# Performance work log

Measured on AMD Instinct MI355X. Metric: run time of the kernel, lower is better.

The kernel has to match this reference:

```python
import jax, jax.numpy as jnp
import numpy as np

NUM_STAB = 0.001  # numerical_stabilizer from relu_kernel_transformation


def relu_kernel(data, proj):
    """ReLU random-feature kernel: data [B,L,H,D], proj [M,D] -> [B,L,H,M]."""
    ratio = 1.0 / jnp.sqrt(jnp.asarray(proj.shape[0], jnp.float32))
    data_dash = ratio * jnp.einsum('blhd,md->blhm', data, proj)
    return jax.nn.relu(data_dash) + NUM_STAB


def setup_inputs() -> dict:
    key = jax.random.key(0)
    k1, k2, k3, k4 = jax.random.split(key, 4)
    B, L, H, D, M = 2, 4096, 8, 64, 256
    return {
        'query': jax.random.normal(k1, (B, L, H, D), jnp.float32),
        'key_t': jax.random.normal(k2, (B, L, H, D), jnp.float32),
        'value': jax.random.normal(k3, (B, L, H, D), jnp.float32),
        'projection_matrix': jax.random.normal(k4, (M, D), jnp.float32),
    }


def reference(query, key_t, value, projection_matrix):
    # Kernel feature maps [B,L,H,M]
    qp = relu_kernel(query, projection_matrix)
    kp = relu_kernel(key_t, projection_matrix)
    # Causal path operates in [L,B,H,*] layout
    qs = jnp.transpose(qp, (1, 0, 2, 3))     # [L,B,H,M]
    ks = jnp.transpose(kp, (1, 0, 2, 3))     # [L,B,H,M]
    vs = jnp.transpose(value, (1, 0, 2, 3))  # [L,B,H,D]

    B, H, M = qs.shape[1], qs.shape[2], qs.shape[3]
    D = vs.shape[3]
    init = (jnp.zeros((B, H, M, D), qs.dtype),  # running sum of k outer v
            jnp.zeros((B, H, M), qs.dtype))     # running sum of k

    def step(carry, inp):
        kv_sum, k_sum = carry
        q, k, v = inp  # [B,H,M], [B,H,M], [B,H,D]
        kv_sum = kv_sum + k[..., None] * v[..., None, :]
        k_sum = k_sum + k
        num = jnp.einsum('bhmd,bhm->bhd', kv_sum, q)  # causal numerator step
        den = jnp.einsum('bhm,bhm->bh', q, k_sum)     # causal denominator step
        return (kv_sum, k_sum), (num, den)

    _, (num, den) = jax.lax.scan(step, init, (qs, ks, vs))  # num [L,B,H,D], den [L,B,H]
    den = den[..., None]
    den = jnp.where(den <= 0.0, jnp.ones_like(den), den)
    out = num / den                      # [L,B,H,D]
    return jnp.transpose(out, (1, 0, 2, 3))  # [B,L,H,D]
```

## Files before the change

### kernel.cpp

```cpp
#include <hip/hip_runtime.h>
#include <hip/hip_bf16.h>


#define B_   2
#define L_   4096
#define H_   8
#define D_   64
#define M_   256
#define T_   128
#define C_   (L_ / T_)
#define NBH  (B_ * H_)
#define RATIO 0.0625f
#define STAB  0.001f
#define SVT  136
#define SQS  72

typedef __attribute__((ext_vector_type(8))) short short8;
typedef __attribute__((ext_vector_type(4))) float floatx4;

#define MFMA16(a, b, c) __builtin_amdgcn_mfma_f32_16x16x32_bf16(a, b, c, 0, 0, 0)

__device__ inline unsigned short f2bf(float x) {
    union { float f; unsigned u; } v; v.f = x;
    unsigned r = v.u + 0x7FFF + ((v.u >> 16) & 1);
    return (unsigned short)(r >> 16);
}
__device__ inline float bf2f(unsigned short b) {
    union { unsigned u; float f; } v; v.u = ((unsigned)b) << 16; return v.f;
}
__device__ inline unsigned pack2bf(float a, float b) {
    __hip_bfloat162 h = __float22bfloat162_rn(make_float2(a, b));
    unsigned u; __builtin_memcpy(&u, &h, 4);
    return u;
}
__device__ inline short8 ldg8_bf(const float* p) {
    float4 a = *(const float4*)p;
    float4 b = *(const float4*)(p + 4);
    short8 r;
    r[0] = (short)f2bf(a.x); r[1] = (short)f2bf(a.y);
    r[2] = (short)f2bf(a.z); r[3] = (short)f2bf(a.w);
    r[4] = (short)f2bf(b.x); r[5] = (short)f2bf(b.y);
    r[6] = (short)f2bf(b.z); r[7] = (short)f2bf(b.w);
    return r;
}
__device__ inline short8 ldg8_bfs(const float* p) {
    float4 a = *(const float4*)p;
    float4 b = *(const float4*)(p + 4);
    short8 r;
    r[0] = (short)f2bf(a.x * RATIO); r[1] = (short)f2bf(a.y * RATIO);
    r[2] = (short)f2bf(a.z * RATIO); r[3] = (short)f2bf(a.w * RATIO);
    r[4] = (short)f2bf(b.x * RATIO); r[5] = (short)f2bf(b.y * RATIO);
    r[6] = (short)f2bf(b.z * RATIO); r[7] = (short)f2bf(b.w * RATIO);
    return r;
}

__global__ __launch_bounds__(512, 2)
void phase1_kernel(const float* __restrict__ key, const float* __restrict__ val,
                   const float* __restrict__ proj,
                   unsigned short* __restrict__ S, float* __restrict__ Z) {
    const int c = blockIdx.x, bh = blockIdx.y;
    const int b = bh / H_, h = bh % H_;
    const int tid = threadIdx.x;
    const int w = tid >> 6, lane = tid & 63;
    const int l15 = lane & 15, quad = lane >> 4;

    __shared__ __align__(16) unsigned short VT[64 * SVT];
    __shared__ __align__(16) unsigned short KpT[128 * SVT];
    __shared__ float zP[8][M_];

    const size_t rowstr = H_ * D_;
    const size_t base = ((size_t)b * L_ + (size_t)c * T_) * rowstr + (size_t)h * D_;

    for (int i = tid; i < T_ * 16; i += 512) {
        int t = i >> 4, d4 = (i & 15) * 4;
        float4 vv = *(const float4*)(val + base + (size_t)t * rowstr + d4);
        VT[(d4 + 0) * SVT + t] = f2bf(vv.x);
        VT[(d4 + 1) * SVT + t] = f2bf(vv.y);
        VT[(d4 + 2) * SVT + t] = f2bf(vv.z);
        VT[(d4 + 3) * SVT + t] = f2bf(vv.w);
    }
    short8 kf[2];
#pragma unroll
    for (int kk = 0; kk < 2; ++kk)
        kf[kk] = ldg8_bfs(key + base + (size_t)(16 * w + l15) * rowstr + kk * 32 + quad * 8);

    const int dtile = w & 3, mq = w >> 2;
    short8 vf[4];
    unsigned short* Sp = S + (size_t)(bh * C_ + c) * (M_ * D_);

    for (int hh = 0; hh < 2; ++hh) {
#pragma unroll
        for (int fgl = 0; fgl < 2; ++fgl) {
            const int fg = 2 * hh + fgl;
#pragma unroll
            for (int ct = 0; ct < 4; ++ct) {
                short8 pf0 = ldg8_bf(proj + (size_t)(fg * 64 + ct * 16 + l15) * D_ + quad * 8);
                short8 pf1 = ldg8_bf(proj + (size_t)(fg * 64 + ct * 16 + l15) * D_ + 32 + quad * 8);
                floatx4 a = {0.f, 0.f, 0.f, 0.f};
                a = MFMA16(kf[0], pf0, a);
                a = MFMA16(kf[1], pf1, a);
                const int mloc = fgl * 64 + ct * 16 + l15;
                float k0 = fmaxf(a[0], 0.f) + STAB;
                float k1 = fmaxf(a[1], 0.f) + STAB;
                float k2 = fmaxf(a[2], 0.f) + STAB;
                float k3 = fmaxf(a[3], 0.f) + STAB;
                uint2 pk; pk.x = pack2bf(k0, k1); pk.y = pack2bf(k2, k3);
                *(uint2*)&KpT[mloc * SVT + 16 * w + quad * 4] = pk;
                float zrow = (k0 + k1) + (k2 + k3);
                zrow += __shfl_xor(zrow, 16, 64);
                zrow += __shfl_xor(zrow, 32, 64);
                if (quad == 0) zP[w][hh * 128 + mloc] = zrow;
            }
        }
        __syncthreads();
        if (hh == 0) {
#pragma unroll
            for (int k4 = 0; k4 < 4; ++k4)
                vf[k4] = *(const short8*)&VT[(16 * dtile + l15) * SVT + k4 * 32 + quad * 8];
        }
#pragma unroll
        for (int ct2 = 0; ct2 < 4; ++ct2) {
            const int mrow = mq * 64 + ct2 * 16 + l15;
            floatx4 acc = {0.f, 0.f, 0.f, 0.f};
#pragma unroll
            for (int k4 = 0; k4 < 4; ++k4) {
                short8 kb = *(const short8*)&KpT[mrow * SVT + k4 * 32 + quad * 8];
                acc = MFMA16(vf[k4], kb, acc);
            }
#pragma unroll
            for (int r = 0; r < 4; ++r)
                Sp[(size_t)(16 * dtile + quad * 4 + r) * M_
                   + hh * 128 + mq * 64 + ct2 * 16 + l15] = f2bf(acc[r]);
        }
        __syncthreads();
    }
    if (tid < M_) {
        float z = 0.f;
#pragma unroll
        for (int ww = 0; ww < 8; ++ww) z += zP[ww][tid];
        Z[(size_t)(bh * C_ + c) * M_ + tid] = z;
    }
}

__global__ __launch_bounds__(256, 4)
void phase2_kernel(unsigned int* __restrict__ S2, float* __restrict__ Z) {
    const int bh = blockIdx.y;
    const int j = blockIdx.x * 256 + threadIdx.x;
    const int NP = M_ * D_ / 2;
    if (j < NP) {
        unsigned int* p = S2 + (size_t)bh * C_ * NP + j;
        unsigned int v[C_];
#pragma unroll
        for (int c = 0; c < C_; ++c) v[c] = p[(size_t)c * NP];
        float r0 = 0.f, r1 = 0.f;
#pragma unroll
        for (int c = 0; c < C_; ++c) {
            unsigned int t = v[c];
            p[(size_t)c * NP] = pack2bf(r0, r1);
            r0 += bf2f((unsigned short)(t & 0xffff));
            r1 += bf2f((unsigned short)(t >> 16));
        }
    } else {
        const int j2 = j - NP;
        if (j2 < M_) {
            float* pz = Z + (size_t)bh * C_ * M_ + j2;
            float v[C_];
#pragma unroll
            for (int c = 0; c < C_; ++c) v[c] = pz[c * M_];
            float run = 0.f;
#pragma unroll
            for (int c = 0; c < C_; ++c) {
                pz[c * M_] = run;
                run += v[c];
            }
        }
    }
}

__global__ __launch_bounds__(512, 2)
void phase3_kernel(const float* __restrict__ q, const float* __restrict__ key,
                   const float* __restrict__ val, const float* __restrict__ proj,
                   const unsigned short* __restrict__ S, const float* __restrict__ Z,
                   float* __restrict__ out) {
    const int c = blockIdx.x, bh = blockIdx.y;
    const int b = bh / H_, h = bh % H_;
    const int tid = threadIdx.x;
    const int w = tid >> 6, lane = tid & 63;
    const int l15 = lane & 15, quad = lane >> 4;

    __shared__ __align__(16) unsigned short KpL[T_ * SVT];
    __shared__ __align__(16) unsigned short VT[64 * SVT];
    __shared__ __align__(16) unsigned short QpS[8 * 16 * SQS];

    const size_t rowstr = H_ * D_;
    const size_t base = ((size_t)b * L_ + (size_t)c * T_) * rowstr + (size_t)h * D_;
    const unsigned short* Sp = S + (size_t)(bh * C_ + c) * (M_ * D_);
    const float* Zp = Z + (size_t)(bh * C_ + c) * M_;

    for (int i = tid; i < T_ * 16; i += 512) {
        int t = i >> 4, d4 = (i & 15) * 4;
        float4 vv = *(const float4*)(val + base + (size_t)t * rowstr + d4);
        VT[(d4 + 0) * SVT + t] = f2bf(vv.x);
        VT[(d4 + 1) * SVT + t] = f2bf(vv.y);
        VT[(d4 + 2) * SVT + t] = f2bf(vv.z);
        VT[(d4 + 3) * SVT + t] = f2bf(vv.w);
    }
    short8 qf[2], kf[2];
#pragma unroll
    for (int kk = 0; kk < 2; ++kk) {
        size_t ro = base + (size_t)(16 * w + l15) * rowstr + kk * 32 + quad * 8;
        qf[kk] = ldg8_bfs(q + ro);
        kf[kk] = ldg8_bfs(key + ro);
    }

    unsigned short* myQp = QpS + w * 16 * SQS;
    floatx4 num[4];
    floatx4 Aacc[8];
#pragma unroll
    for (int dt = 0; dt < 4; ++dt) { floatx4 z4 = {0.f,0.f,0.f,0.f}; num[dt] = z4; }
#pragma unroll
    for (int ct = 0; ct < 8; ++ct) { floatx4 z4 = {0.f,0.f,0.f,0.f}; Aacc[ct] = z4; }
    float dz[4] = {0.f, 0.f, 0.f, 0.f};

    for (int hh = 0; hh < 2; ++hh) {
        short8 qa[4];
#pragma unroll
        for (int fgl = 0; fgl < 2; ++fgl) {
            const int fg = 2 * hh + fgl;
#pragma unroll
            for (int ct = 0; ct < 4; ++ct) {
                const float* pp = proj + (size_t)(fg * 64 + ct * 16 + l15) * D_;
                short8 pf0 = ldg8_bf(pp + quad * 8);
                short8 pf1 = ldg8_bf(pp + 32 + quad * 8);
                floatx4 aq = {0.f, 0.f, 0.f, 0.f};
                aq = MFMA16(qf[0], pf0, aq);
                aq = MFMA16(qf[1], pf1, aq);
                floatx4 ak = {0.f, 0.f, 0.f, 0.f};
                ak = MFMA16(kf[0], pf0, ak);
                ak = MFMA16(kf[1], pf1, ak);
                const int mloc = fgl * 64 + ct * 16 + l15;
                float zv = Zp[hh * 128 + mloc];
#pragma unroll
                for (int r = 0; r < 4; ++r) {
                    float qpv = fmaxf(aq[r], 0.f) + STAB;
                    float kpv = fmaxf(ak[r], 0.f) + STAB;
                    myQp[(quad * 4 + r) * SQS + ct * 16 + l15] = f2bf(qpv);
                    KpL[(size_t)(16 * w + quad * 4 + r) * SVT + mloc] = f2bf(kpv);
                    dz[r] = fmaf(qpv, zv, dz[r]);
                }
            }
#pragma unroll
            for (int kk = 0; kk < 2; ++kk)
                qa[fgl * 2 + kk] = *(const short8*)&myQp[l15 * SQS + kk * 32 + quad * 8];
        }
#pragma unroll
        for (int dt = 0; dt < 4; ++dt)
#pragma unroll
            for (int kc = 0; kc < 4; ++kc) {
                short8 sb = *(const short8*)(Sp + (size_t)(dt * 16 + l15) * M_
                                             + hh * 128 + kc * 32 + quad * 8);
                num[dt] = MFMA16(qa[kc], sb, num[dt]);
            }
        __syncthreads();
#pragma unroll
        for (int ct = 0; ct < 8; ++ct) {
            if (ct <= w) {
#pragma unroll
                for (int kc = 0; kc < 4; ++kc) {
                    short8 kb = *(const short8*)&KpL[(size_t)(ct * 16 + l15) * SVT
                                                     + kc * 32 + quad * 8];
                    Aacc[ct] = MFMA16(qa[kc], kb, Aacc[ct]);
                }
            }
        }
        __syncthreads();
    }
#pragma unroll
    for (int r = 0; r < 4; ++r) {
        dz[r] += __shfl_xor(dz[r], 1, 64);
        dz[r] += __shfl_xor(dz[r], 2, 64);
        dz[r] += __shfl_xor(dz[r], 4, 64);
        dz[r] += __shfl_xor(dz[r], 8, 64);
    }

    unsigned short* AmL = KpL;
    float da[4] = {0.f, 0.f, 0.f, 0.f};
#pragma unroll
    for (int ct = 0; ct < 8; ++ct)
#pragma unroll
        for (int r = 0; r < 4; ++r) {
            float av = Aacc[ct][r];
            if (ct > w || (ct == w && l15 > quad * 4 + r)) av = 0.f;
            AmL[(size_t)(16 * w + quad * 4 + r) * SVT + ct * 16 + l15] = f2bf(av);
            da[r] += av;
        }
#pragma unroll
    for (int r = 0; r < 4; ++r) {
        da[r] += __shfl_xor(da[r], 1, 64);
        da[r] += __shfl_xor(da[r], 2, 64);
        da[r] += __shfl_xor(da[r], 4, 64);
        da[r] += __shfl_xor(da[r], 8, 64);
    }

    for (int k4 = 0; k4 <= (w >> 1); ++k4) {
        short8 am = *(const short8*)&AmL[(size_t)(16 * w + l15) * SVT
                                         + k4 * 32 + quad * 8];
#pragma unroll
        for (int dt = 0; dt < 4; ++dt) {
            short8 vb = *(const short8*)&VT[(dt * 16 + l15) * SVT + k4 * 32 + quad * 8];
            num[dt] = MFMA16(am, vb, num[dt]);
        }
    }

#pragma unroll
    for (int r = 0; r < 4; ++r) {
        float den = da[r] + dz[r];
        if (den <= 0.f) den = 1.f;
        float inv = 1.f / den;
        int t = 16 * w + quad * 4 + r;
#pragma unroll
        for (int dt = 0; dt < 4; ++dt)
            out[base + (size_t)t * rowstr + dt * 16 + l15] = num[dt][r] * inv;
    }
}

extern "C" void kernel_launch(void* const* d_in, const int* in_sizes, int n_in,
                              void* d_out, int out_size, void* d_ws, size_t ws_size,
                              hipStream_t stream) {
    const float* q    = (const float*)d_in[0];
    const float* k    = (const float*)d_in[1];
    const float* v    = (const float*)d_in[2];
    const float* proj = (const float*)d_in[3];
    float* out = (float*)d_out;

    unsigned short* S = (unsigned short*)d_ws;
    float* Z = (float*)(S + (size_t)NBH * C_ * M_ * D_);

    dim3 g1(C_, NBH);
    phase1_kernel<<<g1, dim3(512), 0, stream>>>(k, v, proj, S, Z);
    dim3 g2(33, NBH);
    phase2_kernel<<<g2, dim3(256), 0, stream>>>((unsigned int*)S, Z);
    phase3_kernel<<<g1, dim3(512), 0, stream>>>(q, k, v, proj, S, Z, out);
}
```

Baseline: 190.1 us.

## Split phase kernels across feature/row tiles and reuse key features from workspace

Adds a prep kernel that converts the projection matrix to bf16 once. Phase1 is split across four feature-column blocks with 256 threads each and also stores the bf16 key features to a global workspace. Phase3 is split into two row halves and reads those stored key features and S straight from global memory instead of recomputing key features and staging them in LDS. This raises block count and parallelism and cuts redundant projection work, in exchange for extra global traffic and a workspace-size-dependent fallback path.

```diff
diff --git a/kernel.cpp b/kernel.cpp
--- a/kernel.cpp
+++ b/kernel.cpp
@@ -13,7 +13,6 @@
 #define RATIO 0.0625f
 #define STAB  0.001f
 #define SVT  136
-#define SQS  72
 
 typedef __attribute__((ext_vector_type(8))) short short8;
 typedef __attribute__((ext_vector_type(4))) float floatx4;
@@ -54,24 +53,34 @@
     return r;
 }
 
-__global__ __launch_bounds__(512, 2)
+__global__ __launch_bounds__(256, 4)
+void prep_kernel(const float* __restrict__ proj, unsigned short* __restrict__ Pbf) {
+    int i = blockIdx.x * 256 + threadIdx.x;
+    float4 v = *(const float4*)(proj + (size_t)i * 4);
+    uint2 p; p.x = pack2bf(v.x, v.y); p.y = pack2bf(v.z, v.w);
+    *(uint2*)(Pbf + (size_t)i * 4) = p;
+}
+
+template<bool WKPG>
+__global__ __launch_bounds__(256, 4)
 void phase1_kernel(const float* __restrict__ key, const float* __restrict__ val,
-                   const float* __restrict__ proj,
-                   unsigned short* __restrict__ S, float* __restrict__ Z) {
-    const int c = blockIdx.x, bh = blockIdx.y;
+                   const unsigned short* __restrict__ Pbf,
+                   unsigned short* __restrict__ S, float* __restrict__ Z,
+                   unsigned short* __restrict__ Kpg) {
+    const int c = blockIdx.x, bh = blockIdx.y, mq = blockIdx.z;
     const int b = bh / H_, h = bh % H_;
     const int tid = threadIdx.x;
     const int w = tid >> 6, lane = tid & 63;
     const int l15 = lane & 15, quad = lane >> 4;
 
     __shared__ __align__(16) unsigned short VT[64 * SVT];
-    __shared__ __align__(16) unsigned short KpT[128 * SVT];
-    __shared__ float zP[8][M_];
+    __shared__ __align__(16) unsigned short KpT[64 * SVT];
+    __shared__ float zP[4][64];
 
     const size_t rowstr = H_ * D_;
     const size_t base = ((size_t)b * L_ + (size_t)c * T_) * rowstr + (size_t)h * D_;
 
-    for (int i = tid; i < T_ * 16; i += 512) {
+    for (int i = tid; i < T_ * 16; i += 256) {
         int t = i >> 4, d4 = (i & 15) * 4;
         float4 vv = *(const float4*)(val + base + (size_t)t * rowstr + d4);
         VT[(d4 + 0) * SVT + t] = f2bf(vv.x);
@@ -79,67 +88,70 @@
         VT[(d4 + 2) * SVT + t] = f2bf(vv.z);
         VT[(d4 + 3) * SVT + t] = f2bf(vv.w);
     }
-    short8 kf[2];
-#pragma unroll
-    for (int kk = 0; kk < 2; ++kk)
-        kf[kk] = ldg8_bfs(key + base + (size_t)(16 * w + l15) * rowstr + kk * 32 + quad * 8);
-
-    const int dtile = w & 3, mq = w >> 2;
+    short8 kf[2][2];
+#pragma unroll
+    for (int rt = 0; rt < 2; ++rt)
+#pragma unroll
+        for (int kk = 0; kk < 2; ++kk)
+            kf[rt][kk] = ldg8_bfs(key + base + (size_t)(32 * w + rt * 16 + l15) * rowstr
+                                  + kk * 32 + quad * 8);
+
+    unsigned short* Kpc = Kpg + (size_t)(bh * C_ + c) * (T_ * M_);
+#pragma unroll
+    for (int ct = 0; ct < 4; ++ct) {
+        const int mloc = ct * 16 + l15;
+        const int m = mq * 64 + mloc;
+        short8 pf0 = *(const short8*)(Pbf + (size_t)m * D_ + quad * 8);
+        short8 pf1 = *(const short8*)(Pbf + (size_t)m * D_ + 32 + quad * 8);
+        float zsum = 0.f;
+#pragma unroll
+        for (int rt = 0; rt < 2; ++rt) {
+            floatx4 a = {0.f, 0.f, 0.f, 0.f};
+            a = MFMA16(kf[rt][0], pf0, a);
+            a = MFMA16(kf[rt][1], pf1, a);
+            unsigned short u[4];
+#pragma unroll
+            for (int r = 0; r < 4; ++r) {
+                float kpf = fmaxf(a[r], 0.f) + STAB;
+                u[r] = f2bf(kpf);
+                zsum += kpf;
+            }
+            uint2 pk;
+            pk.x = (unsigned)u[0] | ((unsigned)u[1] << 16);
+            pk.y = (unsigned)u[2] | ((unsigned)u[3] << 16);
+            *(uint2*)&KpT[mloc * SVT + 32 * w + rt * 16 + quad * 4] = pk;
+            if (WKPG) {
+#pragma unroll
+                for (int r = 0; r < 4; ++r)
+                    Kpc[(size_t)(32 * w + rt * 16 + quad * 4 + r) * M_ + m] = u[r];
+            }
+        }
+        zsum += __shfl_xor(zsum, 16, 64);
+        zsum += __shfl_xor(zsum, 32, 64);
+        if (quad == 0) zP[w][mloc] = zsum;
+    }
+    __syncthreads();
+
     short8 vf[4];
+#pragma unroll
+    for (int k4 = 0; k4 < 4; ++k4)
+        vf[k4] = *(const short8*)&VT[(16 * w + l15) * SVT + k4 * 32 + quad * 8];
     unsigned short* Sp = S + (size_t)(bh * C_ + c) * (M_ * D_);
-
-    for (int hh = 0; hh < 2; ++hh) {
-#pragma unroll
-        for (int fgl = 0; fgl < 2; ++fgl) {
-            const int fg = 2 * hh + fgl;
-#pragma unroll
-            for (int ct = 0; ct < 4; ++ct) {
-                short8 pf0 = ldg8_bf(proj + (size_t)(fg * 64 + ct * 16 + l15) * D_ + quad * 8);
-                short8 pf1 = ldg8_bf(proj + (size_t)(fg * 64 + ct * 16 + l15) * D_ + 32 + quad * 8);
-                floatx4 a = {0.f, 0.f, 0.f, 0.f};
-                a = MFMA16(kf[0], pf0, a);
-                a = MFMA16(kf[1], pf1, a);
-                const int mloc = fgl * 64 + ct * 16 + l15;
-                float k0 = fmaxf(a[0], 0.f) + STAB;
-                float k1 = fmaxf(a[1], 0.f) + STAB;
-                float k2 = fmaxf(a[2], 0.f) + STAB;
-                float k3 = fmaxf(a[3], 0.f) + STAB;
-                uint2 pk; pk.x = pack2bf(k0, k1); pk.y = pack2bf(k2, k3);
-                *(uint2*)&KpT[mloc * SVT + 16 * w + quad * 4] = pk;
-                float zrow = (k0 + k1) + (k2 + k3);
-                zrow += __shfl_xor(zrow, 16, 64);
-                zrow += __shfl_xor(zrow, 32, 64);
-                if (quad == 0) zP[w][hh * 128 + mloc] = zrow;
-            }
-        }
-        __syncthreads();
-        if (hh == 0) {
-#pragma unroll
-            for (int k4 = 0; k4 < 4; ++k4)
-                vf[k4] = *(const short8*)&VT[(16 * dtile + l15) * SVT + k4 * 32 + quad * 8];
-        }
-#pragma unroll
-        for (int ct2 = 0; ct2 < 4; ++ct2) {
-            const int mrow = mq * 64 + ct2 * 16 + l15;
-            floatx4 acc = {0.f, 0.f, 0.f, 0.f};
-#pragma unroll
-            for (int k4 = 0; k4 < 4; ++k4) {
-                short8 kb = *(const short8*)&KpT[mrow * SVT + k4 * 32 + quad * 8];
-                acc = MFMA16(vf[k4], kb, acc);
-            }
-#pragma unroll
-            for (int r = 0; r < 4; ++r)
-                Sp[(size_t)(16 * dtile + quad * 4 + r) * M_
-                   + hh * 128 + mq * 64 + ct2 * 16 + l15] = f2bf(acc[r]);
-        }
-        __syncthreads();
-    }
-    if (tid < M_) {
-        float z = 0.f;
-#pragma unroll
-        for (int ww = 0; ww < 8; ++ww) z += zP[ww][tid];
-        Z[(size_t)(bh * C_ + c) * M_ + tid] = z;
-    }
+#pragma unroll
+    for (int ct2 = 0; ct2 < 4; ++ct2) {
+        floatx4 acc = {0.f, 0.f, 0.f, 0.f};
+#pragma unroll
+        for (int k4 = 0; k4 < 4; ++k4) {
+            short8 kb = *(const short8*)&KpT[(ct2 * 16 + l15) * SVT + k4 * 32 + quad * 8];
+            acc = MFMA16(vf[k4], kb, acc);
+        }
+#pragma unroll
+        for (int r = 0; r < 4; ++r)
+            Sp[(size_t)(16 * w + quad * 4 + r) * M_ + mq * 64 + ct2 * 16 + l15] = f2bf(acc[r]);
+    }
+    if (tid < 64)
+        Z[(size_t)(bh * C_ + c) * M_ + mq * 64 + tid] =
+            zP[0][tid] + zP[1][tid] + zP[2][tid] + zP[3][tid];
 }
 
 __global__ __launch_bounds__(256, 4)
@@ -177,11 +189,149 @@
     }
 }
 
+__global__ __launch_bounds__(256, 4)
+void phase3_kernel(const float* __restrict__ q, const float* __restrict__ val,
+                   const unsigned short* __restrict__ Pbf,
+                   const unsigned short* __restrict__ S, const float* __restrict__ Z,
+                   const unsigned short* __restrict__ Kpg,
+                   float* __restrict__ out) {
+    const int c = blockIdx.x, bh = blockIdx.y, uh = blockIdx.z;
+    const int b = bh / H_, h = bh % H_;
+    const int tid = threadIdx.x;
+    const int w = tid >> 6, lane = tid & 63;
+    const int l15 = lane & 15, quad = lane >> 4;
+    const int rt_glob = uh * 4 + w;
+
+    __shared__ __align__(16) unsigned short VT[64 * SVT];
+    __shared__ __align__(16) unsigned short QA[4][16 * SVT];
+
+    const size_t rowstr = H_ * D_;
+    const size_t base = ((size_t)b * L_ + (size_t)c * T_) * rowstr + (size_t)h * D_;
+    const unsigned short* Sp = S + (size_t)(bh * C_ + c) * (M_ * D_);
+    const float* Zp = Z + (size_t)(bh * C_ + c) * M_;
+    const unsigned short* Kpc = Kpg + (size_t)(bh * C_ + c) * (T_ * M_);
+
+    for (int i = tid; i < T_ * 16; i += 256) {
+        int t = i >> 4, d4 = (i & 15) * 4;
+        float4 vv = *(const float4*)(val + base + (size_t)t * rowstr + d4);
+        VT[(d4 + 0) * SVT + t] = f2bf(vv.x);
+        VT[(d4 + 1) * SVT + t] = f2bf(vv.y);
+        VT[(d4 + 2) * SVT + t] = f2bf(vv.z);
+        VT[(d4 + 3) * SVT + t] = f2bf(vv.w);
+    }
+    short8 qf[2];
+#pragma unroll
+    for (int kk = 0; kk < 2; ++kk)
+        qf[kk] = ldg8_bfs(q + base + (size_t)(uh * 64 + 16 * w + l15) * rowstr
+                          + kk * 32 + quad * 8);
+
+    unsigned short* myQ = QA[w];
+    floatx4 num[4];
+    floatx4 Aacc[8];
+#pragma unroll
+    for (int dt = 0; dt < 4; ++dt) { floatx4 z4 = {0.f,0.f,0.f,0.f}; num[dt] = z4; }
+#pragma unroll
+    for (int ct = 0; ct < 8; ++ct) { floatx4 z4 = {0.f,0.f,0.f,0.f}; Aacc[ct] = z4; }
+    float dz[4] = {0.f, 0.f, 0.f, 0.f};
+
+    for (int hh = 0; hh < 2; ++hh) {
+#pragma unroll
+        for (int ct = 0; ct < 8; ++ct) {
+            const int m = hh * 128 + ct * 16 + l15;
+            short8 pf0 = *(const short8*)(Pbf + (size_t)m * D_ + quad * 8);
+            short8 pf1 = *(const short8*)(Pbf + (size_t)m * D_ + 32 + quad * 8);
+            floatx4 aq = {0.f, 0.f, 0.f, 0.f};
+            aq = MFMA16(qf[0], pf0, aq);
+            aq = MFMA16(qf[1], pf1, aq);
+            float zv = Zp[m];
+#pragma unroll
+            for (int r = 0; r < 4; ++r) {
+                float qpv = fmaxf(aq[r], 0.f) + STAB;
+                myQ[(quad * 4 + r) * SVT + ct * 16 + l15] = f2bf(qpv);
+                dz[r] = fmaf(qpv, zv, dz[r]);
+            }
+        }
+        short8 qa[4];
+#pragma unroll
+        for (int kc = 0; kc < 4; ++kc)
+            qa[kc] = *(const short8*)&myQ[l15 * SVT + kc * 32 + quad * 8];
+#pragma unroll
+        for (int dt = 0; dt < 4; ++dt)
+#pragma unroll
+            for (int kc = 0; kc < 4; ++kc) {
+                short8 sb = *(const short8*)(Sp + (size_t)(dt * 16 + l15) * M_
+                                             + hh * 128 + kc * 32 + quad * 8);
+                num[dt] = MFMA16(qa[kc], sb, num[dt]);
+            }
+#pragma unroll
+        for (int ct = 0; ct < 8; ++ct) {
+            if (ct <= rt_glob) {
+#pragma unroll
+                for (int kc = 0; kc < 4; ++kc) {
+                    short8 kb = *(const short8*)(Kpc + (size_t)(ct * 16 + l15) * M_
+                                                 + hh * 128 + kc * 32 + quad * 8);
+                    Aacc[ct] = MFMA16(qa[kc], kb, Aacc[ct]);
+                }
+            }
+        }
+    }
+#pragma unroll
+    for (int r = 0; r < 4; ++r) {
+        dz[r] += __shfl_xor(dz[r], 1, 64);
+        dz[r] += __shfl_xor(dz[r], 2, 64);
+        dz[r] += __shfl_xor(dz[r], 4, 64);
+        dz[r] += __shfl_xor(dz[r], 8, 64);
+    }
+
+    float da[4] = {0.f, 0.f, 0.f, 0.f};
+    const int ctmax = rt_glob | 1;
+#pragma unroll
+    for (int ct = 0; ct < 8; ++ct) {
+        if (ct > ctmax) continue;
+#pragma unroll
+        for (int r = 0; r < 4; ++r) {
+            float av = Aacc[ct][r];
+            if (ct > rt_glob || (ct == rt_glob && l15 > quad * 4 + r)) av = 0.f;
+            myQ[(quad * 4 + r) * SVT + ct * 16 + l15] = f2bf(av);
+            da[r] += av;
+        }
+    }
+#pragma unroll
+    for (int r = 0; r < 4; ++r) {
+        da[r] += __shfl_xor(da[r], 1, 64);
+        da[r] += __shfl_xor(da[r], 2, 64);
+        da[r] += __shfl_xor(da[r], 4, 64);
+        da[r] += __shfl_xor(da[r], 8, 64);
+    }
+    __syncthreads();
+
+    for (int k4 = 0; k4 <= (rt_glob >> 1); ++k4) {
+        short8 am = *(const short8*)&myQ[l15 * SVT + k4 * 32 + quad * 8];
+#pragma unroll
+        for (int dt = 0; dt < 4; ++dt) {
+            short8 vb = *(const short8*)&VT[(dt * 16 + l15) * SVT + k4 * 32 + quad * 8];
+            num[dt] = MFMA16(am, vb, num[dt]);
+        }
+    }
+
+#pragma unroll
+    for (int r = 0; r < 4; ++r) {
+        float den = da[r] + dz[r];
+        if (den <= 0.f) den = 1.f;
+        float inv = 1.f / den;
+        int t = uh * 64 + 16 * w + quad * 4 + r;
+#pragma unroll
+        for (int dt = 0; dt < 4; ++dt)
+            out[base + (size_t)t * rowstr + dt * 16 + l15] = num[dt][r] * inv;
+    }
+}
+
+#define SQS  72
 __global__ __launch_bounds__(512, 2)
-void phase3_kernel(const float* __restrict__ q, const float* __restrict__ key,
-                   const float* __restrict__ val, const float* __restrict__ proj,
-                   const unsigned short* __restrict__ S, const float* __restrict__ Z,
-                   float* __restrict__ out) {
+void phase3_fb(const float* __restrict__ q, const float* __restrict__ key,
+               const float* __restrict__ val, const float* __restrict__ proj,
+               const unsigned short* __restrict__ S, const float* __restrict__ Z,
+               float* __restrict__ out) {
     const int c = blockIdx.x, bh = blockIdx.y;
     const int b = bh / H_, h = bh % H_;
     const int tid = threadIdx.x;
@@ -212,7 +362,6 @@
         qf[kk] = ldg8_bfs(q + ro);
         kf[kk] = ldg8_bfs(key + ro);
     }
-
     unsigned short* myQp = QpS + w * 16 * SQS;
     floatx4 num[4];
     floatx4 Aacc[8];
@@ -282,7 +431,6 @@
         dz[r] += __shfl_xor(dz[r], 4, 64);
         dz[r] += __shfl_xor(dz[r], 8, 64);
     }
-
     unsigned short* AmL = KpL;
     float da[4] = {0.f, 0.f, 0.f, 0.f};
 #pragma unroll
@@ -301,17 +449,14 @@
         da[r] += __shfl_xor(da[r], 4, 64);
         da[r] += __shfl_xor(da[r], 8, 64);
     }
-
     for (int k4 = 0; k4 <= (w >> 1); ++k4) {
-        short8 am = *(const short8*)&AmL[(size_t)(16 * w + l15) * SVT
-                                         + k4 * 32 + quad * 8];
+        short8 am = *(const short8*)&AmL[(size_t)(16 * w + l15) * SVT + k4 * 32 + quad * 8];
 #pragma unroll
         for (int dt = 0; dt < 4; ++dt) {
             short8 vb = *(const short8*)&VT[(dt * 16 + l15) * SVT + k4 * 32 + quad * 8];
             num[dt] = MFMA16(am, vb, num[dt]);
         }
     }
-
 #pragma unroll
     for (int r = 0; r < 4; ++r) {
         float den = da[r] + dz[r];
@@ -333,12 +478,27 @@
     const float* proj = (const float*)d_in[3];
     float* out = (float*)d_out;
 
+    const size_t nS = (size_t)NBH * C_ * D_ * M_;
+    const size_t nZ = (size_t)NBH * C_ * M_;
+    const size_t nK = (size_t)NBH * C_ * T_ * M_;
     unsigned short* S = (unsigned short*)d_ws;
-    float* Z = (float*)(S + (size_t)NBH * C_ * M_ * D_);
-
-    dim3 g1(C_, NBH);
-    phase1_kernel<<<g1, dim3(512), 0, stream>>>(k, v, proj, S, Z);
+    float* Z = (float*)(S + nS);
+    const size_t need_big = nS * 2 + nZ * 4 + nK * 2 + (size_t)M_ * D_ * 2;
+    const bool big = ws_size >= need_big;
+
+    unsigned short* Kpg = (unsigned short*)(Z + nZ);
+    unsigned short* Pbf = big ? (Kpg + nK) : (unsigned short*)(Z + nZ);
+
+    prep_kernel<<<dim3(16), dim3(256), 0, stream>>>(proj, Pbf);
+    dim3 g1(C_, NBH, 4);
+    if (big)
+        phase1_kernel<true><<<g1, dim3(256), 0, stream>>>(k, v, Pbf, S, Z, Kpg);
+    else
+        phase1_kernel<false><<<g1, dim3(256), 0, stream>>>(k, v, Pbf, S, Z, S );
     dim3 g2(33, NBH);
     phase2_kernel<<<g2, dim3(256), 0, stream>>>((unsigned int*)S, Z);
-    phase3_kernel<<<g1, dim3(512), 0, stream>>>(q, k, v, proj, S, Z, out);
-}
+    if (big)
+        phase3_kernel<<<dim3(C_, NBH, 2), dim3(256), 0, stream>>>(q, v, Pbf, S, Z, Kpg, out);
+    else
+        phase3_fb<<<dim3(C_, NBH), dim3(512), 0, stream>>>(q, k, v, proj, S, Z, out);
+}
```

After: 195.2 us. +2.7%, slower.

## Replace chunk-parallel state build plus prefix pass with fused sequential scan kernel

Applied to the files above, without the earlier changes.

Adds a prep kernel that converts key, the transposed value chunks and the projection to bf16 once. It then replaces the per-chunk state kernel and the separate prefix-sum kernel with one scan kernel. Each block owns an (M-slice, D-half) tile and walks all chunks in order, writing exclusive prefix states directly, with double-buffered LDS and prefetch of the next key chunk. The aim is to remove the extra read and write of the full bf16 state array and the repeated fp32 conversions. The cost is a serial 32-step dependency chain per block, and phase3 now reads V fragments from global memory instead of LDS.

```diff
diff --git a/kernel.cpp b/kernel.cpp
--- a/kernel.cpp
+++ b/kernel.cpp
@@ -25,23 +25,10 @@
     unsigned r = v.u + 0x7FFF + ((v.u >> 16) & 1);
     return (unsigned short)(r >> 16);
 }
-__device__ inline float bf2f(unsigned short b) {
-    union { unsigned u; float f; } v; v.u = ((unsigned)b) << 16; return v.f;
-}
 __device__ inline unsigned pack2bf(float a, float b) {
     __hip_bfloat162 h = __float22bfloat162_rn(make_float2(a, b));
     unsigned u; __builtin_memcpy(&u, &h, 4);
     return u;
-}
-__device__ inline short8 ldg8_bf(const float* p) {
-    float4 a = *(const float4*)p;
-    float4 b = *(const float4*)(p + 4);
-    short8 r;
-    r[0] = (short)f2bf(a.x); r[1] = (short)f2bf(a.y);
-    r[2] = (short)f2bf(a.z); r[3] = (short)f2bf(a.w);
-    r[4] = (short)f2bf(b.x); r[5] = (short)f2bf(b.y);
-    r[6] = (short)f2bf(b.z); r[7] = (short)f2bf(b.w);
-    return r;
 }
 __device__ inline short8 ldg8_bfs(const float* p) {
     float4 a = *(const float4*)p;
@@ -54,24 +41,27 @@
     return r;
 }
 
-__global__ __launch_bounds__(512, 2)
-void phase1_kernel(const float* __restrict__ key, const float* __restrict__ val,
-                   const float* __restrict__ proj,
-                   unsigned short* __restrict__ S, float* __restrict__ Z) {
+__global__ __launch_bounds__(256, 2)
+void prep_kernel(const float* __restrict__ key, const float* __restrict__ val,
+                 const float* __restrict__ proj,
+                 unsigned short* __restrict__ kbf, unsigned short* __restrict__ VTg,
+                 unsigned short* __restrict__ Pbf) {
     const int c = blockIdx.x, bh = blockIdx.y;
     const int b = bh / H_, h = bh % H_;
     const int tid = threadIdx.x;
-    const int w = tid >> 6, lane = tid & 63;
-    const int l15 = lane & 15, quad = lane >> 4;
-
     __shared__ __align__(16) unsigned short VT[64 * SVT];
-    __shared__ __align__(16) unsigned short KpT[128 * SVT];
-    __shared__ float zP[8][M_];
 
     const size_t rowstr = H_ * D_;
     const size_t base = ((size_t)b * L_ + (size_t)c * T_) * rowstr + (size_t)h * D_;
 
-    for (int i = tid; i < T_ * 16; i += 512) {
+    for (int i = tid; i < T_ * 16; i += 256) {
+        int t = i >> 4, dd = (i & 15) * 4;
+        float4 kv = *(const float4*)(key + base + (size_t)t * rowstr + dd);
+        uint2 o; o.x = pack2bf(kv.x * RATIO, kv.y * RATIO);
+        o.y = pack2bf(kv.z * RATIO, kv.w * RATIO);
+        *(uint2*)(kbf + base + (size_t)t * rowstr + dd) = o;
+    }
+    for (int i = tid; i < T_ * 16; i += 256) {
         int t = i >> 4, d4 = (i & 15) * 4;
         float4 vv = *(const float4*)(val + base + (size_t)t * rowstr + d4);
         VT[(d4 + 0) * SVT + t] = f2bf(vv.x);
@@ -79,107 +69,127 @@
         VT[(d4 + 2) * SVT + t] = f2bf(vv.z);
         VT[(d4 + 3) * SVT + t] = f2bf(vv.w);
     }
-    short8 kf[2];
-#pragma unroll
-    for (int kk = 0; kk < 2; ++kk)
-        kf[kk] = ldg8_bfs(key + base + (size_t)(16 * w + l15) * rowstr + kk * 32 + quad * 8);
-
-    const int dtile = w & 3, mq = w >> 2;
-    short8 vf[4];
-    unsigned short* Sp = S + (size_t)(bh * C_ + c) * (M_ * D_);
-
-    for (int hh = 0; hh < 2; ++hh) {
-#pragma unroll
-        for (int fgl = 0; fgl < 2; ++fgl) {
-            const int fg = 2 * hh + fgl;
-#pragma unroll
-            for (int ct = 0; ct < 4; ++ct) {
-                short8 pf0 = ldg8_bf(proj + (size_t)(fg * 64 + ct * 16 + l15) * D_ + quad * 8);
-                short8 pf1 = ldg8_bf(proj + (size_t)(fg * 64 + ct * 16 + l15) * D_ + 32 + quad * 8);
+    __syncthreads();
+    unsigned short* vout = VTg + ((size_t)bh * C_ + c) * (D_ * T_);
+    for (int i = tid; i < D_ * 16; i += 256) {
+        int d = i >> 4, tt = (i & 15) * 8;
+        *(uint4*)(vout + d * T_ + tt) = *(const uint4*)&VT[d * SVT + tt];
+    }
+    if (c == 0) {
+        int i = bh * 256 + tid;
+        float4 pv = *(const float4*)(proj + (size_t)i * 4);
+        uint2 o; o.x = pack2bf(pv.x, pv.y); o.y = pack2bf(pv.z, pv.w);
+        *(uint2*)(Pbf + (size_t)i * 4) = o;
+    }
+}
+
+__global__ __launch_bounds__(256, 2)
+void scan_kernel(const unsigned short* __restrict__ kbf,
+                 const unsigned short* __restrict__ VTg,
+                 const unsigned short* __restrict__ Pbf,
+                 unsigned short* __restrict__ S, float* __restrict__ Z) {
+    const int mq = blockIdx.x, bh = blockIdx.y, dh = blockIdx.z;
+    const int b = bh / H_, h = bh % H_;
+    const int tid = threadIdx.x;
+    const int w = tid >> 6, lane = tid & 63;
+    const int l15 = lane & 15, quad = lane >> 4;
+    const int dt = w & 1, ct2 = w >> 1;
+
+    __shared__ __align__(16) unsigned short KpT[2][32 * SVT];
+    __shared__ float zP[2][4][32];
+
+    const size_t rowstr = H_ * D_;
+
+    short8 pf[2][2];
+#pragma unroll
+    for (int ct = 0; ct < 2; ++ct)
+#pragma unroll
+        for (int kk = 0; kk < 2; ++kk)
+            pf[ct][kk] = *(const short8*)(Pbf + (size_t)(mq * 32 + ct * 16 + l15) * D_
+                                          + kk * 32 + quad * 8);
+
+    floatx4 acc = {0.f, 0.f, 0.f, 0.f};
+    float zreg = 0.f;
+
+    short8 kf[2][2];
+#pragma unroll
+    for (int rt = 0; rt < 2; ++rt)
+#pragma unroll
+        for (int kk = 0; kk < 2; ++kk)
+            kf[rt][kk] = *(const short8*)(kbf + ((size_t)b * L_) * rowstr + (size_t)h * D_
+                                          + (size_t)(32 * w + rt * 16 + l15) * rowstr
+                                          + kk * 32 + quad * 8);
+
+    const int vrow = dh * 32 + dt * 16 + l15;
+    const int drow0 = dh * 32 + dt * 16 + quad * 4;
+    const int mcol = mq * 32 + ct2 * 16 + l15;
+
+    for (int c = 0; c < C_; ++c) {
+        const int buf = c & 1;
+        float zpart[2] = {0.f, 0.f};
+#pragma unroll
+        for (int rt = 0; rt < 2; ++rt)
+#pragma unroll
+            for (int ct = 0; ct < 2; ++ct) {
                 floatx4 a = {0.f, 0.f, 0.f, 0.f};
-                a = MFMA16(kf[0], pf0, a);
-                a = MFMA16(kf[1], pf1, a);
-                const int mloc = fgl * 64 + ct * 16 + l15;
+                a = MFMA16(kf[rt][0], pf[ct][0], a);
+                a = MFMA16(kf[rt][1], pf[ct][1], a);
                 float k0 = fmaxf(a[0], 0.f) + STAB;
                 float k1 = fmaxf(a[1], 0.f) + STAB;
                 float k2 = fmaxf(a[2], 0.f) + STAB;
                 float k3 = fmaxf(a[3], 0.f) + STAB;
+                zpart[ct] += (k0 + k1) + (k2 + k3);
                 uint2 pk; pk.x = pack2bf(k0, k1); pk.y = pack2bf(k2, k3);
-                *(uint2*)&KpT[mloc * SVT + 16 * w + quad * 4] = pk;
-                float zrow = (k0 + k1) + (k2 + k3);
-                zrow += __shfl_xor(zrow, 16, 64);
-                zrow += __shfl_xor(zrow, 32, 64);
-                if (quad == 0) zP[w][hh * 128 + mloc] = zrow;
+                *(uint2*)&KpT[buf][(ct * 16 + l15) * SVT + 32 * w + rt * 16 + quad * 4] = pk;
             }
-        }
+#pragma unroll
+        for (int ct = 0; ct < 2; ++ct) {
+            float z = zpart[ct];
+            z += __shfl_xor(z, 16, 64);
+            z += __shfl_xor(z, 32, 64);
+            if (quad == 0) zP[buf][w][ct * 16 + l15] = z;
+        }
+        if (c + 1 < C_) {
+            const size_t kb2 = ((size_t)b * L_ + (size_t)(c + 1) * T_) * rowstr + (size_t)h * D_;
+#pragma unroll
+            for (int rt = 0; rt < 2; ++rt)
+#pragma unroll
+                for (int kk = 0; kk < 2; ++kk)
+                    kf[rt][kk] = *(const short8*)(kbf + kb2
+                                                  + (size_t)(32 * w + rt * 16 + l15) * rowstr
+                                                  + kk * 32 + quad * 8);
+        }
+        const unsigned short* vbase = VTg + ((size_t)bh * C_ + c) * (D_ * T_);
+        short8 vf[4];
+#pragma unroll
+        for (int k4 = 0; k4 < 4; ++k4)
+            vf[k4] = *(const short8*)(vbase + (size_t)vrow * T_ + k4 * 32 + quad * 8);
+
         __syncthreads();
-        if (hh == 0) {
-#pragma unroll
-            for (int k4 = 0; k4 < 4; ++k4)
-                vf[k4] = *(const short8*)&VT[(16 * dtile + l15) * SVT + k4 * 32 + quad * 8];
-        }
-#pragma unroll
-        for (int ct2 = 0; ct2 < 4; ++ct2) {
-            const int mrow = mq * 64 + ct2 * 16 + l15;
-            floatx4 acc = {0.f, 0.f, 0.f, 0.f};
-#pragma unroll
-            for (int k4 = 0; k4 < 4; ++k4) {
-                short8 kb = *(const short8*)&KpT[mrow * SVT + k4 * 32 + quad * 8];
-                acc = MFMA16(vf[k4], kb, acc);
-            }
-#pragma unroll
-            for (int r = 0; r < 4; ++r)
-                Sp[(size_t)(16 * dtile + quad * 4 + r) * M_
-                   + hh * 128 + mq * 64 + ct2 * 16 + l15] = f2bf(acc[r]);
-        }
-        __syncthreads();
-    }
-    if (tid < M_) {
-        float z = 0.f;
-#pragma unroll
-        for (int ww = 0; ww < 8; ++ww) z += zP[ww][tid];
-        Z[(size_t)(bh * C_ + c) * M_ + tid] = z;
-    }
-}
-
-__global__ __launch_bounds__(256, 4)
-void phase2_kernel(unsigned int* __restrict__ S2, float* __restrict__ Z) {
-    const int bh = blockIdx.y;
-    const int j = blockIdx.x * 256 + threadIdx.x;
-    const int NP = M_ * D_ / 2;
-    if (j < NP) {
-        unsigned int* p = S2 + (size_t)bh * C_ * NP + j;
-        unsigned int v[C_];
-#pragma unroll
-        for (int c = 0; c < C_; ++c) v[c] = p[(size_t)c * NP];
-        float r0 = 0.f, r1 = 0.f;
-#pragma unroll
-        for (int c = 0; c < C_; ++c) {
-            unsigned int t = v[c];
-            p[(size_t)c * NP] = pack2bf(r0, r1);
-            r0 += bf2f((unsigned short)(t & 0xffff));
-            r1 += bf2f((unsigned short)(t >> 16));
-        }
-    } else {
-        const int j2 = j - NP;
-        if (j2 < M_) {
-            float* pz = Z + (size_t)bh * C_ * M_ + j2;
-            float v[C_];
-#pragma unroll
-            for (int c = 0; c < C_; ++c) v[c] = pz[c * M_];
-            float run = 0.f;
-#pragma unroll
-            for (int c = 0; c < C_; ++c) {
-                pz[c * M_] = run;
-                run += v[c];
-            }
+
+        unsigned short* Sp = S + ((size_t)bh * C_ + c) * (M_ * D_);
+#pragma unroll
+        for (int r = 0; r < 4; ++r)
+            Sp[(size_t)(drow0 + r) * M_ + mcol] = f2bf(acc[r]);
+        if (dh == 0 && w == 0 && lane < 32) {
+            float zs = zP[buf][0][lane] + zP[buf][1][lane]
+                     + zP[buf][2][lane] + zP[buf][3][lane];
+            Z[((size_t)bh * C_ + c) * M_ + mq * 32 + lane] = zreg;
+            zreg += zs;
+        }
+#pragma unroll
+        for (int k4 = 0; k4 < 4; ++k4) {
+            short8 kb = *(const short8*)&KpT[buf][(ct2 * 16 + l15) * SVT + k4 * 32 + quad * 8];
+            acc = MFMA16(vf[k4], kb, acc);
         }
     }
 }
 
 __global__ __launch_bounds__(512, 2)
-void phase3_kernel(const float* __restrict__ q, const float* __restrict__ key,
-                   const float* __restrict__ val, const float* __restrict__ proj,
+void phase3_kernel(const float* __restrict__ q,
+                   const unsigned short* __restrict__ kbf,
+                   const unsigned short* __restrict__ VTg,
+                   const unsigned short* __restrict__ Pbf,
                    const unsigned short* __restrict__ S, const float* __restrict__ Z,
                    float* __restrict__ out) {
     const int c = blockIdx.x, bh = blockIdx.y;
@@ -189,28 +199,20 @@
     const int l15 = lane & 15, quad = lane >> 4;
 
     __shared__ __align__(16) unsigned short KpL[T_ * SVT];
-    __shared__ __align__(16) unsigned short VT[64 * SVT];
     __shared__ __align__(16) unsigned short QpS[8 * 16 * SQS];
 
     const size_t rowstr = H_ * D_;
     const size_t base = ((size_t)b * L_ + (size_t)c * T_) * rowstr + (size_t)h * D_;
     const unsigned short* Sp = S + (size_t)(bh * C_ + c) * (M_ * D_);
     const float* Zp = Z + (size_t)(bh * C_ + c) * M_;
-
-    for (int i = tid; i < T_ * 16; i += 512) {
-        int t = i >> 4, d4 = (i & 15) * 4;
-        float4 vv = *(const float4*)(val + base + (size_t)t * rowstr + d4);
-        VT[(d4 + 0) * SVT + t] = f2bf(vv.x);
-        VT[(d4 + 1) * SVT + t] = f2bf(vv.y);
-        VT[(d4 + 2) * SVT + t] = f2bf(vv.z);
-        VT[(d4 + 3) * SVT + t] = f2bf(vv.w);
-    }
+    const unsigned short* Vc = VTg + ((size_t)bh * C_ + c) * (D_ * T_);
+
     short8 qf[2], kf[2];
 #pragma unroll
     for (int kk = 0; kk < 2; ++kk) {
         size_t ro = base + (size_t)(16 * w + l15) * rowstr + kk * 32 + quad * 8;
         qf[kk] = ldg8_bfs(q + ro);
-        kf[kk] = ldg8_bfs(key + ro);
+        kf[kk] = *(const short8*)(kbf + ro);
     }
 
     unsigned short* myQp = QpS + w * 16 * SQS;
@@ -229,9 +231,9 @@
             const int fg = 2 * hh + fgl;
 #pragma unroll
             for (int ct = 0; ct < 4; ++ct) {
-                const float* pp = proj + (size_t)(fg * 64 + ct * 16 + l15) * D_;
-                short8 pf0 = ldg8_bf(pp + quad * 8);
-                short8 pf1 = ldg8_bf(pp + 32 + quad * 8);
+                const unsigned short* pp = Pbf + (size_t)(fg * 64 + ct * 16 + l15) * D_;
+                short8 pf0 = *(const short8*)(pp + quad * 8);
+                short8 pf1 = *(const short8*)(pp + 32 + quad * 8);
                 floatx4 aq = {0.f, 0.f, 0.f, 0.f};
                 aq = MFMA16(qf[0], pf0, aq);
                 aq = MFMA16(qf[1], pf1, aq);
@@ -307,7 +309,8 @@
                                          + k4 * 32 + quad * 8];
 #pragma unroll
         for (int dt = 0; dt < 4; ++dt) {
-            short8 vb = *(const short8*)&VT[(dt * 16 + l15) * SVT + k4 * 32 + quad * 8];
+            short8 vb = *(const short8*)(Vc + (size_t)(dt * 16 + l15) * T_
+                                         + k4 * 32 + quad * 8);
             num[dt] = MFMA16(am, vb, num[dt]);
         }
     }
@@ -333,12 +336,17 @@
     const float* proj = (const float*)d_in[3];
     float* out = (float*)d_out;
 
-    unsigned short* S = (unsigned short*)d_ws;
-    float* Z = (float*)(S + (size_t)NBH * C_ * M_ * D_);
-
-    dim3 g1(C_, NBH);
-    phase1_kernel<<<g1, dim3(512), 0, stream>>>(k, v, proj, S, Z);
-    dim3 g2(33, NBH);
-    phase2_kernel<<<g2, dim3(256), 0, stream>>>((unsigned int*)S, Z);
-    phase3_kernel<<<g1, dim3(512), 0, stream>>>(q, k, v, proj, S, Z, out);
-}
+    const size_t nS = (size_t)NBH * C_ * D_ * M_;
+    const size_t nZ = (size_t)NBH * C_ * M_;
+    const size_t nK = (size_t)B_ * L_ * H_ * D_;
+    const size_t nV = (size_t)NBH * C_ * D_ * T_;
+    unsigned short* S   = (unsigned short*)d_ws;
+    float*          Z   = (float*)(S + nS);
+    unsigned short* kbf = (unsigned short*)(Z + nZ);
+    unsigned short* VTg = kbf + nK;
+    unsigned short* Pbf = VTg + nV;
+
+    prep_kernel<<<dim3(C_, NBH), dim3(256), 0, stream>>>(k, v, proj, kbf, VTg, Pbf);
+    scan_kernel<<<dim3(8, NBH, 2), dim3(256), 0, stream>>>(kbf, VTg, Pbf, S, Z);
+    phase3_kernel<<<dim3(C_, NBH), dim3(512), 0, stream>>>(q, kbf, VTg, Pbf, S, Z, out);
+}
```

Result: slower. 196.2 us (+3.2%).
